# Kernel optimization log

Hardware: AMD Instinct MI355X
Metric: run time of the kernel (lower is better)

Reference implementation:

```python
import jax, jax.numpy as jnp
import numpy as np

jax.config.update("jax_enable_x64", True)

VOCAB = 50257
GAMMA = 0.25
CW = 4              # context_width
HASH_KEY = 15485863
Z_CENTER = 2.0
TEMP = 2.0
P = 2147483647      # Mersenne prime 2**31 - 1 used as hash modulus
GREEN_SIZE = int(GAMMA * VOCAB)


def setup_inputs() -> dict:
    key = jax.random.key(0)
    k1, k2 = jax.random.split(key)
    B, S = 512, 8192
    token_ids = jax.random.randint(k1, (B, S), 0, VOCAB, dtype=jnp.int64)
    lengths = jax.random.randint(k2, (B,), 0, S, dtype=jnp.int64)
    dummy = jnp.zeros((1,), dtype=jnp.float32)  # mirrors non-trainable self._dummy
    return {"token_ids": token_ids, "lengths": lengths, "dummy": dummy}


def reference(token_ids, lengths, dummy):
    # KGW z-score detector, fully vectorized over (batch, seq).
    # Context hash: h_t = hash_key * prod_{i=1..CW} (tok_{t-i}+1)  (mod P)
    # Token t is "green" iff ((h_t * (tok_t+1)) mod P) mod VOCAB < gamma*VOCAB.
    tok = token_ids.astype(jnp.int64) + 1  # +1 avoids zero in the product
    B, S = tok.shape
    h = jnp.full((B, S), HASH_KEY % P, dtype=jnp.int64)
    for i in range(1, CW + 1):  # small fixed loop over context_width
        prev = jnp.pad(tok, ((0, 0), (i, 0)), constant_values=1)[:, :S]
        h = (h * prev) % P
    is_green = ((h * tok) % P) % VOCAB < GREEN_SIZE  # (B, S) bool

    pos = jnp.arange(S)
    valid = (pos[None, :] >= CW) & (pos[None, :] < lengths[:, None])
    count = jnp.sum(is_green & valid, axis=1).astype(jnp.float32)

    T = jnp.maximum(lengths - CW, 1).astype(jnp.float32)  # number of scored tokens
    z = (count - GAMMA * T) / jnp.sqrt(GAMMA * (1.0 - GAMMA) * T)
    reward = jax.nn.sigmoid((z - Z_CENTER) / TEMP)
    # sequences shorter than context_width+1 get reward 0
    reward = jnp.where(lengths >= CW + 1, reward, 0.0).astype(jnp.float32)
    return reward + 0.0 * jnp.sum(dummy)
```

## Files before the change

### kernel.cpp

```cpp
#include <hip/hip_runtime.h>


#define VOCAB 50257u
#define GREEN_SIZE 12564u
#define CW 4
#define HASH_KEY 15485863u
#define P31 2147483647u
#define SMAX 8192

__device__ __forceinline__ unsigned int mulmodP(unsigned int a, unsigned int b) {
    unsigned long long x = (unsigned long long)a * (unsigned long long)b;
    unsigned int y = (unsigned int)(x & P31) + (unsigned int)(x >> 31);
    y = (y & P31) + (y >> 31);
    if (y >= P31) y -= P31;
    return y;
}

__global__ __launch_bounds__(256) void kgw_fused(
        const void* __restrict__ tokens, const void* __restrict__ lengths,
        float* __restrict__ out, int S) {
    __shared__ int s_tok[SMAX];
    __shared__ int s_red[4];
    __shared__ int s_any;

    const int b   = blockIdx.x;
    const int tid = threadIdx.x;

    if (tid == 0) s_any = 0;
    __syncthreads();
    if (((const unsigned int*)tokens)[2 * tid + 1] != 0u) atomicOr(&s_any, 1);
    __syncthreads();
    const int is64 = (s_any == 0);

    long long L;
    if (is64) L = ((const long long*)lengths)[b];
    else      L = (long long)((const int*)lengths)[b];
    const int Li = (int)L;

    if (Li < CW + 1) {
        if (tid == 0) out[b] = 0.0f;
        return;
    }

    if (is64) {
        const longlong2* tp2 = (const longlong2*)((const long long*)tokens + (size_t)b * (size_t)S);
        const int npair = Li >> 1;
        for (int i = tid; i < npair; i += 256) {
            longlong2 v = tp2[i];
            s_tok[2 * i]     = (int)v.x + 1;
            s_tok[2 * i + 1] = (int)v.y + 1;
        }
        if ((Li & 1) && tid == 0)
            s_tok[Li - 1] = (int)((const long long*)tokens)[(size_t)b * (size_t)S + Li - 1] + 1;
    } else {
        const int* tp = (const int*)tokens + (size_t)b * (size_t)S;
        const int nq = Li >> 2;
        const int4* tp4 = (const int4*)tp;
        for (int i = tid; i < nq; i += 256) {
            int4 v = tp4[i];
            s_tok[4 * i]     = v.x + 1;
            s_tok[4 * i + 1] = v.y + 1;
            s_tok[4 * i + 2] = v.z + 1;
            s_tok[4 * i + 3] = v.w + 1;
        }
        for (int t = 4 * nq + tid; t < Li; t += 256) s_tok[t] = tp[t] + 1;
    }
    __syncthreads();

    int cnt = 0;
    for (int t = CW + tid; t < Li; t += 256) {
        unsigned int h = HASH_KEY;
        h = mulmodP(h, (unsigned int)s_tok[t - 1]);
        h = mulmodP(h, (unsigned int)s_tok[t - 2]);
        h = mulmodP(h, (unsigned int)s_tok[t - 3]);
        h = mulmodP(h, (unsigned int)s_tok[t - 4]);
        unsigned int g = mulmodP(h, (unsigned int)s_tok[t]);
        cnt += ((g % VOCAB) < GREEN_SIZE) ? 1 : 0;
    }

    for (int off = 32; off > 0; off >>= 1) cnt += __shfl_down(cnt, off, 64);
    const int lane = tid & 63, wave = tid >> 6;
    if (lane == 0) s_red[wave] = cnt;
    __syncthreads();

    if (tid == 0) {
        const float count = (float)(s_red[0] + s_red[1] + s_red[2] + s_red[3]);
        const float T = (float)(Li - CW);
        const float z = (count - 0.25f * T) / sqrtf(0.1875f * T);
        const float x = (z - 2.0f) * 0.5f;
        out[b] = 1.0f / (1.0f + expf(-x));
    }
}

extern "C" void kernel_launch(void* const* d_in, const int* in_sizes, int n_in,
                              void* d_out, int out_size, void* d_ws, size_t ws_size,
                              hipStream_t stream) {
    const void* tokens  = d_in[0];
    const void* lengths = d_in[1];
    float* out = (float*)d_out;

    const int B = out_size;
    const int S = in_sizes[0] / B;

    kgw_fused<<<B, 256, 0, stream>>>(tokens, lengths, out, S);
}
```

Measured before the change: 15.01 us.

## Split each sequence across eight blocks and reduce partial counts in second kernel

Each sequence is now split into eight chunks handled by separate blocks, which stage only their chunk plus a small halo in shared memory. Per-chunk green counts go to a workspace buffer, and a second small kernel sums them and computes the sigmoid reward. This is meant to fix load imbalance and low parallelism across 512 blocks with varying lengths, and it also loads only the low 32-bit words of int64 tokens and defers the full mod reduction. The cost is a second kernel launch, a workspace round trip, and CHUNK depending on S being a multiple of 8 with S/8 no larger than 1024.

Result: slower. 16.70 us (+11.2%).

```diff
diff --git a/kernel.cpp b/kernel.cpp
--- a/kernel.cpp
+++ b/kernel.cpp
@@ -6,25 +6,28 @@
 #define CW 4
 #define HASH_KEY 15485863u
 #define P31 2147483647u
-#define SMAX 8192
+#define NSPLIT 8
+#define CHUNK_MAX 1024
+#define STAGE_MAX (CHUNK_MAX + CW)
 
-__device__ __forceinline__ unsigned int mulmodP(unsigned int a, unsigned int b) {
+__device__ __forceinline__ unsigned int mulmodP_lazy(unsigned int a, unsigned int b) {
     unsigned long long x = (unsigned long long)a * (unsigned long long)b;
     unsigned int y = (unsigned int)(x & P31) + (unsigned int)(x >> 31);
-    y = (y & P31) + (y >> 31);
-    if (y >= P31) y -= P31;
-    return y;
+    return (y & P31) + (y >> 31);
 }
 
-__global__ __launch_bounds__(256) void kgw_fused(
+__global__ __launch_bounds__(256) void kgw_partial(
         const void* __restrict__ tokens, const void* __restrict__ lengths,
-        float* __restrict__ out, int S) {
-    __shared__ int s_tok[SMAX];
+        int* __restrict__ partial, int S) {
+    __shared__ int s_tok[STAGE_MAX];
     __shared__ int s_red[4];
     __shared__ int s_any;
 
-    const int b   = blockIdx.x;
+    const int bid = blockIdx.x;
+    const int b   = bid >> 3;
+    const int p   = bid & (NSPLIT - 1);
     const int tid = threadIdx.x;
+    const int CHUNK = S >> 3;
 
     if (tid == 0) s_any = 0;
     __syncthreads();
@@ -32,64 +35,73 @@
     __syncthreads();
     const int is64 = (s_any == 0);
 
-    long long L;
-    if (is64) L = ((const long long*)lengths)[b];
-    else      L = (long long)((const int*)lengths)[b];
-    const int Li = (int)L;
+    const int Li = is64 ? (int)((const long long*)lengths)[b]
+                        : ((const int*)lengths)[b];
 
-    if (Li < CW + 1) {
-        if (tid == 0) out[b] = 0.0f;
-        return;
-    }
-
-    if (is64) {
-        const longlong2* tp2 = (const longlong2*)((const long long*)tokens + (size_t)b * (size_t)S);
-        const int npair = Li >> 1;
-        for (int i = tid; i < npair; i += 256) {
-            longlong2 v = tp2[i];
-            s_tok[2 * i]     = (int)v.x + 1;
-            s_tok[2 * i + 1] = (int)v.y + 1;
-        }
-        if ((Li & 1) && tid == 0)
-            s_tok[Li - 1] = (int)((const long long*)tokens)[(size_t)b * (size_t)S + Li - 1] + 1;
-    } else {
-        const int* tp = (const int*)tokens + (size_t)b * (size_t)S;
-        const int nq = Li >> 2;
-        const int4* tp4 = (const int4*)tp;
-        for (int i = tid; i < nq; i += 256) {
-            int4 v = tp4[i];
-            s_tok[4 * i]     = v.x + 1;
-            s_tok[4 * i + 1] = v.y + 1;
-            s_tok[4 * i + 2] = v.z + 1;
-            s_tok[4 * i + 3] = v.w + 1;
-        }
-        for (int t = 4 * nq + tid; t < Li; t += 256) s_tok[t] = tp[t] + 1;
-    }
-    __syncthreads();
+    int t0 = p * CHUNK; if (t0 < CW) t0 = CW;
+    int t1 = (p + 1) * CHUNK; if (t1 > Li) t1 = Li;
 
     int cnt = 0;
-    for (int t = CW + tid; t < Li; t += 256) {
-        unsigned int h = HASH_KEY;
-        h = mulmodP(h, (unsigned int)s_tok[t - 1]);
-        h = mulmodP(h, (unsigned int)s_tok[t - 2]);
-        h = mulmodP(h, (unsigned int)s_tok[t - 3]);
-        h = mulmodP(h, (unsigned int)s_tok[t - 4]);
-        unsigned int g = mulmodP(h, (unsigned int)s_tok[t]);
-        cnt += ((g % VOCAB) < GREEN_SIZE) ? 1 : 0;
+    if (t0 < t1) {
+        const int base = t0 - CW;
+        const int n = t1 - base;
+        if (is64) {
+            const unsigned int* tp = (const unsigned int*)tokens
+                                     + 2 * ((size_t)b * (size_t)S + (size_t)base);
+            for (int i = tid; i < n; i += 256) s_tok[i] = (int)tp[2 * i] + 1;
+        } else {
+            const int* tp = (const int*)tokens + (size_t)b * (size_t)S + base;
+            for (int i = tid; i < n; i += 256) s_tok[i] = tp[i] + 1;
+        }
+        __syncthreads();
+
+        for (int t = t0 + tid; t < t1; t += 256) {
+            const int j = t - base;
+            unsigned int h = HASH_KEY;
+            h = mulmodP_lazy(h, (unsigned int)s_tok[j - 1]);
+            h = mulmodP_lazy(h, (unsigned int)s_tok[j - 2]);
+            h = mulmodP_lazy(h, (unsigned int)s_tok[j - 3]);
+            h = mulmodP_lazy(h, (unsigned int)s_tok[j - 4]);
+            unsigned int g = mulmodP_lazy(h, (unsigned int)s_tok[j]);
+            g = (g & P31) + (g >> 31);
+            if (g >= P31) g -= P31;
+            cnt += ((g % VOCAB) < GREEN_SIZE) ? 1 : 0;
+        }
     }
 
     for (int off = 32; off > 0; off >>= 1) cnt += __shfl_down(cnt, off, 64);
-    const int lane = tid & 63, wave = tid >> 6;
-    if (lane == 0) s_red[wave] = cnt;
+    if ((tid & 63) == 0) s_red[tid >> 6] = cnt;
     __syncthreads();
+    if (tid == 0) partial[bid] = s_red[0] + s_red[1] + s_red[2] + s_red[3];
+}
 
-    if (tid == 0) {
-        const float count = (float)(s_red[0] + s_red[1] + s_red[2] + s_red[3]);
+__global__ __launch_bounds__(256) void kgw_final(
+        const void* __restrict__ tokens, const void* __restrict__ lengths,
+        const int* __restrict__ partial, float* __restrict__ out, int B) {
+    __shared__ int s_any;
+    if (threadIdx.x == 0) s_any = 0;
+    __syncthreads();
+    if (((const unsigned int*)tokens)[2 * threadIdx.x + 1] != 0u) atomicOr(&s_any, 1);
+    __syncthreads();
+    const int is64 = (s_any == 0);
+
+    const int b = blockIdx.x * 256 + threadIdx.x;
+    if (b >= B) return;
+
+    const int Li = is64 ? (int)((const long long*)lengths)[b]
+                        : ((const int*)lengths)[b];
+
+    const int4* pp = (const int4*)(partial + b * NSPLIT);
+    const int4 a = pp[0], c = pp[1];
+    const int cnt = a.x + a.y + a.z + a.w + c.x + c.y + c.z + c.w;
+
+    float r = 0.0f;
+    if (Li >= CW + 1) {
         const float T = (float)(Li - CW);
-        const float z = (count - 0.25f * T) / sqrtf(0.1875f * T);
-        const float x = (z - 2.0f) * 0.5f;
-        out[b] = 1.0f / (1.0f + expf(-x));
+        const float z = ((float)cnt - 0.25f * T) / sqrtf(0.1875f * T);
+        r = 1.0f / (1.0f + expf(-(z - 2.0f) * 0.5f));
     }
+    out[b] = r;
 }
 
 extern "C" void kernel_launch(void* const* d_in, const int* in_sizes, int n_in,
@@ -97,10 +109,12 @@
                               hipStream_t stream) {
     const void* tokens  = d_in[0];
     const void* lengths = d_in[1];
-    float* out = (float*)d_out;
+    float* out   = (float*)d_out;
+    int* partial = (int*)d_ws;
 
     const int B = out_size;
     const int S = in_sizes[0] / B;
 
-    kgw_fused<<<B, 256, 0, stream>>>(tokens, lengths, out, S);
+    kgw_partial<<<B * NSPLIT, 256, 0, stream>>>(tokens, lengths, partial, S);
+    kgw_final<<<(B + 255) / 256, 256, 0, stream>>>(tokens, lengths, partial, out, B);
 }
```
